# Kernel tuning notes

Hardware: AMD Instinct MI355X
Metric: run time of the kernel (lower is better)

## Reference

```python
import jax, jax.numpy as jnp
import numpy as np

B, M, N = 2, 256, 256
K, P, Q, D = 8, 512, 512, 64
R, Pp, Qp, Dp = 128, 512, 512, 64
TEMP = float(np.sqrt(Dp))  # softmax temperature = sqrt(D')


def _xavier(key, shape):
    # xavier_uniform over last two dims (fan_in, fan_out), matching torch init on (K, d, D)
    fan_in, fan_out = shape[-2], shape[-1]
    lim = float(np.sqrt(6.0 / (fan_in + fan_out)))
    return jax.random.uniform(key, shape, jnp.float32, -lim, lim)


def setup_inputs() -> dict:
    key = jax.random.key(0)
    ks = jax.random.split(key, 9)
    return {
        "z": jax.random.normal(ks[0], (B, M, N, R), jnp.float32),
        "y_q": jax.random.normal(ks[1], (B, N, Qp), jnp.float32),
        "x_k": jax.random.normal(ks[2], (B, M, Pp), jnp.float32),
        "Theta_x": _xavier(ks[3], (K, P, D)),
        "Theta_y": _xavier(ks[4], (K, Q, D)),
        "Lam_x": _xavier(ks[5], (K, Pp, Dp)),
        "Lam_y": _xavier(ks[6], (K, Qp, Dp)),
        "Lam_zx": _xavier(ks[7], (K, R, Dp)),
        "Lam_zy": _xavier(ks[8], (K, R, Dp)),
    }


def reference(z, y_q, x_k, Theta_x, Theta_y, Lam_x, Lam_y, Lam_zx, Lam_zy):
    # --- mixed attention scores ---
    xt = jnp.einsum('bmp,kpd->bkmd', x_k, Lam_x)          # [B,K,M,D']
    yt = jnp.einsum('bnq,kqd->bknd', y_q, Lam_y)          # [B,K,N,D']
    r = jnp.einsum('bkmd,bknd->bkmn', xt, yt)             # pairwise term
    zy = jnp.einsum('bmnr,krd->bkmnd', z, Lam_zy)         # [B,K,M,N,D'] (large)
    r = r + jnp.einsum('bkmnd,bkmd->bkmn', zy, xt)
    r = r + jnp.einsum('bknd,bmnr,krd->bkmn', yt, z, Lam_zx)
    # --- generalised convolution (mask=None, bias=False) ---
    a = jax.nn.softmax(r / TEMP, axis=-2)                 # softmax over M (column-wise)
    xv = jnp.einsum('bmp,kpd->bkmd', x_k, Theta_x)        # value projection
    y = jnp.einsum('bkmn,bkmd,kqd->bnq', a, xv, Theta_y)  # [B,N,Q]
    return y
```

## Files before the change

### kernel.cpp

```cpp
#include <hip/hip_runtime.h>
#include <hip/hip_bf16.h>

#define LOG2E_OVER_T 0.18033688011112042f

typedef __attribute__((ext_vector_type(8))) short short8;
typedef __attribute__((ext_vector_type(4))) float f32x4;
typedef unsigned short ushort_t;
typedef unsigned long long ull_t;

#define MFMA16(a, b, c) __builtin_amdgcn_mfma_f32_16x16x32_bf16(a, b, c, 0, 0, 0)

__device__ __forceinline__ ushort_t f2bf(float f) {
    union { float f; unsigned u; } v; v.f = f;
    unsigned r = (v.u + 0x7fffu + ((v.u >> 16) & 1u)) >> 16;
    return (ushort_t)r;
}

__device__ __forceinline__ void gload16(const float* g, float* l) {
    __builtin_amdgcn_global_load_lds(
        (const __attribute__((address_space(1))) void*)g,
        (__attribute__((address_space(3))) void*)l, 16, 0, 0);
}

__device__ __forceinline__ void split8(const float4 a, const float4 b,
                                       short8& hi, short8& lo)
{
    union { float f[8]; unsigned u[8]; } Z;
    Z.f[0] = a.x; Z.f[1] = a.y; Z.f[2] = a.z; Z.f[3] = a.w;
    Z.f[4] = b.x; Z.f[5] = b.y; Z.f[6] = b.z; Z.f[7] = b.w;
    union { unsigned u[4]; short8 s; } H, L;
    #pragma unroll
    for (int i = 0; i < 4; i++) {
        const unsigned u0 = Z.u[2 * i], u1 = Z.u[2 * i + 1];
        H.u[i] = __builtin_amdgcn_perm(u1, u0, 0x07060302u);
        union { unsigned u; float f; } h0, h1;
        h0.u = u0 & 0xffff0000u; h1.u = u1 & 0xffff0000u;
        union { float f; unsigned u; } l0, l1;
        l0.f = Z.f[2 * i] - h0.f; l1.f = Z.f[2 * i + 1] - h1.f;
        L.u[i] = __builtin_amdgcn_perm(l1.u, l0.u, 0x07060302u);
    }
    hi = H.s; lo = L.s;
}

__device__ __forceinline__ void mfma_core64(
    const ushort_t* __restrict__ Ag, int lda,
    const ushort_t* __restrict__ Btg, int ldb,
    int ksteps, f32x4 acc[2][2])
{
    __shared__ __align__(16) ushort_t As[64 * 40];
    __shared__ __align__(16) ushort_t Bs[64 * 40];
    const int t = threadIdx.x;
    const int srow = t >> 2, skc = (t & 3) * 8;
    const int lane = t & 63, w = t >> 6;
    const int wr = w >> 1, wc = w & 1;
    const int fr = lane & 15, kg = lane >> 4;
    const int aoff = (wr * 32 + fr) * 40 + kg * 8;
    const int boff = (wc * 32 + fr) * 40 + kg * 8;
    const long arow = (long)srow * lda + skc;
    const long brow = (long)srow * ldb + skc;

    short8 ra = *(const short8*)(Ag + arow);
    short8 rb = *(const short8*)(Btg + brow);
    for (int kt = 0; kt < ksteps; kt++) {
        __syncthreads();
        *(short8*)&As[srow * 40 + skc] = ra;
        *(short8*)&Bs[srow * 40 + skc] = rb;
        __syncthreads();
        if (kt + 1 < ksteps) {
            ra = *(const short8*)(Ag + arow + (kt + 1) * 32);
            rb = *(const short8*)(Btg + brow + (kt + 1) * 32);
        }
        short8 a0 = *(const short8*)&As[aoff];
        short8 a1 = *(const short8*)&As[aoff + 16 * 40];
        short8 b0 = *(const short8*)&Bs[boff];
        short8 b1 = *(const short8*)&Bs[boff + 16 * 40];
        acc[0][0] = MFMA16(a0, b0, acc[0][0]);
        acc[0][1] = MFMA16(a0, b1, acc[0][1]);
        acc[1][0] = MFMA16(a1, b0, acc[1][0]);
        acc[1][1] = MFMA16(a1, b1, acc[1][1]);
    }
}

__device__ __forceinline__ void zero_acc(f32x4 acc[2][2]) {
    const f32x4 z4 = {0.f, 0.f, 0.f, 0.f};
    acc[0][0] = z4; acc[0][1] = z4; acc[1][0] = z4; acc[1][1] = z4;
}

__global__ __launch_bounds__(256)
void convert_kernel(const float* __restrict__ x_k, const float* __restrict__ y_q,
                    const float* __restrict__ Lam_x, const float* __restrict__ Theta_x,
                    const float* __restrict__ Lam_y, const float* __restrict__ Lam_zy,
                    const float* __restrict__ Lam_zx, const float* __restrict__ Theta_y,
                    ushort_t* __restrict__ xkb, ushort_t* __restrict__ yqb,
                    ushort_t* __restrict__ WxTb, ushort_t* __restrict__ WyTb,
                    ushort_t* __restrict__ Zyb, ushort_t* __restrict__ Zxb,
                    ushort_t* __restrict__ TyTb, float* __restrict__ ssum)
{
    int i = blockIdx.x * 256 + threadIdx.x;
    if (i < 262144) { xkb[i] = f2bf(x_k[i]); return; }
    i -= 262144;
    if (i < 262144) { yqb[i] = f2bf(y_q[i]); return; }
    i -= 262144;
    if (i < 524288) {
        const int k = i >> 16, rem = i & 65535, dc = rem >> 9, p = i & 511;
        const float v = (dc < 64) ? Lam_x[((long)k * 512 + p) * 64 + dc]
                                  : Theta_x[((long)k * 512 + p) * 64 + dc - 64];
        WxTb[i] = f2bf(v); return;
    }
    i -= 524288;
    if (i < 262144) {
        const int k = i >> 15, d = (i >> 9) & 63, p = i & 511;
        WyTb[i] = f2bf(Lam_y[((long)k * 512 + p) * 64 + d]); return;
    }
    i -= 262144;
    if (i < 65536) { Zyb[i] = f2bf(Lam_zy[i]); return; }
    i -= 65536;
    if (i < 65536) { Zxb[i] = f2bf(Lam_zx[i]); return; }
    i -= 65536;
    if (i < 262144) {
        const int q = i >> 9, kd = i & 511, k = kd >> 6, d = kd & 63;
        TyTb[i] = f2bf(Theta_y[((long)k * 512 + q) * 64 + d]); return;
    }
    i -= 262144;
    ssum[i] = 0.f;
}

__global__ __launch_bounds__(256)
void proj_kernel(const ushort_t* __restrict__ xkb, const ushort_t* __restrict__ yqb,
                 const ushort_t* __restrict__ WxTb, const ushort_t* __restrict__ WyTb,
                 ushort_t* __restrict__ xtb, ushort_t* __restrict__ ytb,
                 ushort_t* __restrict__ xvTb)
{
    const int side = blockIdx.z;
    const int bx = blockIdx.x, by = blockIdx.y;
    if (side == 1 && bx >= 8) return;
    f32x4 acc[2][2]; zero_acc(acc);
    const int t = threadIdx.x, lane = t & 63, w = t >> 6;
    const int wr = w >> 1, wc = w & 1, fr = lane & 15, kg = lane >> 4;

    if (side == 0) {
        mfma_core64(xkb + (long)(by * 64) * 512, 512,
                    WxTb + (long)(bx * 64) * 512, 512, 16, acc);
        const int k = bx >> 1, isxv = bx & 1;
        #pragma unroll
        for (int mi = 0; mi < 2; mi++)
        #pragma unroll
        for (int ni = 0; ni < 2; ni++) {
            const int grow0 = by * 64 + wr * 32 + mi * 16 + kg * 4;
            const int b = grow0 >> 8, m0 = grow0 & 255;
            const int d = wc * 32 + ni * 16 + fr;
            if (!isxv) {
                #pragma unroll
                for (int j = 0; j < 4; j++)
                    xtb[(((long)(b * 8 + k)) * 256 + m0 + j) * 64 + d] = f2bf(acc[mi][ni][j]);
            } else {
                ull_t pk = (ull_t)f2bf(acc[mi][ni][0])
                         | ((ull_t)f2bf(acc[mi][ni][1]) << 16)
                         | ((ull_t)f2bf(acc[mi][ni][2]) << 32)
                         | ((ull_t)f2bf(acc[mi][ni][3]) << 48);
                *(ull_t*)&xvTb[(((long)(b * 8 + k)) * 64 + d) * 256 + m0] = pk;
            }
        }
    } else {
        mfma_core64(yqb + (long)(by * 64) * 512, 512,
                    WyTb + (long)(bx * 64) * 512, 512, 16, acc);
        const int k = bx;
        #pragma unroll
        for (int mi = 0; mi < 2; mi++)
        #pragma unroll
        for (int ni = 0; ni < 2; ni++)
        #pragma unroll
        for (int j = 0; j < 4; j++) {
            const int grow = by * 64 + wr * 32 + mi * 16 + kg * 4 + j;
            const int b = grow >> 8, n = grow & 255;
            const int d = wc * 32 + ni * 16 + fr;
            ytb[(((long)(b * 8 + k)) * 256 + n) * 64 + d] = f2bf(acc[mi][ni][j]);
        }
    }
}

__global__ __launch_bounds__(256)
void step2_kernel(const ushort_t* __restrict__ xtb, const ushort_t* __restrict__ ytb,
                  const ushort_t* __restrict__ Zyb, const ushort_t* __restrict__ Zxb,
                  ushort_t* __restrict__ wzyb, ushort_t* __restrict__ wzxb,
                  float* __restrict__ t1)
{
    const int bz = blockIdx.x;
    const int t = threadIdx.x, lane = t & 63, w = t >> 6;
    const int wr = w >> 1, wc = w & 1, fr = lane & 15, kg = lane >> 4;

    if (bz < 256) {
        const int which = bz >> 7, idx = bz & 127;
        const int bk = idx >> 3, tile = idx & 7, mt = tile >> 1, nt = tile & 1;
        const int k = bk & 7, b = bk >> 3;
        const ushort_t* Ag  = (which ? ytb : xtb) + ((long)bk * 256 + mt * 64) * 64;
        const ushort_t* Btg = (which ? Zxb : Zyb) + ((long)k * 128 + nt * 64) * 64;
        ushort_t* C = which ? wzxb : wzyb;
        f32x4 acc[2][2]; zero_acc(acc);
        mfma_core64(Ag, 64, Btg, 64, 2, acc);
        #pragma unroll
        for (int mi = 0; mi < 2; mi++)
        #pragma unroll
        for (int ni = 0; ni < 2; ni++)
        #pragma unroll
        for (int j = 0; j < 4; j++) {
            const int m_glob = mt * 64 + wr * 32 + mi * 16 + kg * 4 + j;
            const int r_glob = nt * 64 + wc * 32 + ni * 16 + fr;
            C[(((long)b * 256 + m_glob) * 8 + k) * 128 + r_glob] = f2bf(acc[mi][ni][j]);
        }
    } else {
        const int idx = bz - 256;
        const int bk = idx >> 4, tile = idx & 15, nt2 = tile >> 2, mt2 = tile & 3;
        f32x4 acc[2][2]; zero_acc(acc);
        mfma_core64(ytb + ((long)bk * 256 + nt2 * 64) * 64, 64,
                    xtb + ((long)bk * 256 + mt2 * 64) * 64, 64, 2, acc);
        #pragma unroll
        for (int mi = 0; mi < 2; mi++)
        #pragma unroll
        for (int ni = 0; ni < 2; ni++)
        #pragma unroll
        for (int j = 0; j < 4; j++) {
            const int n_glob = nt2 * 64 + wr * 32 + mi * 16 + kg * 4 + j;
            const int m_glob = mt2 * 64 + wc * 32 + ni * 16 + fr;
            t1[((long)bk * 256 + n_glob) * 256 + m_glob] = acc[mi][ni][j];
        }
    }
}

__global__ __launch_bounds__(256)
void fused_score(const float* __restrict__ z,
                 const ushort_t* __restrict__ wzyb, const ushort_t* __restrict__ wzxb,
                 const float* __restrict__ t1, ushort_t* __restrict__ Et,
                 float* __restrict__ ssum)
{
    const int nt = blockIdx.x, mt = blockIdx.y, b = blockIdx.z;
    const int nbase = nt * 16, m0 = mt * 8;
    __shared__ __align__(16) float zs[8192];
    __shared__ float sc[4][8][8][17];

    const int tid = threadIdx.x;
    const int lane = tid & 63, w = tid >> 6;
    const int fr = lane & 15, kg = lane >> 4;
    const int f8 = fr & 7;

    const int js   = w * 512 + lane;
    for (int c = 0; c < 2; c++) {
        const int n0c = nbase + c * 8;

        #pragma unroll
        for (int i = 0; i < 8; i++) {
            const int j   = js + i * 64;
            const int row = j >> 5;
            const int m_l = row >> 3, n_l = row & 7;
            const int sl  = (j & 31) ^ ((m_l ^ n_l) & 7);
            const float* src = z + (((long)b * 256 + m0 + m_l) * 256 + n0c + n_l) * 128 + sl * 4;
            gload16(src, &zs[(w * 8 + i) * 256]);
        }
        __syncthreads();

        #pragma unroll
        for (int m = 0; m < 8; m++) {
            const int row = m * 8 + f8;
            const int key = (m ^ f8) & 7;
            const int s0 = (w * 8 + kg * 2) ^ key, s1 = (w * 8 + kg * 2 + 1) ^ key;
            const float4 za = *(const float4*)&zs[row * 128 + s0 * 4];
            const float4 zb = *(const float4*)&zs[row * 128 + s1 * 4];
            const short8 wv = *(const short8*)(wzyb
                + (((long)b * 256 + m0 + m) * 8 + f8) * 128 + w * 32 + kg * 8);
            short8 hi, lo;
            split8(za, zb, hi, lo);
            f32x4 acc = {0.f, 0.f, 0.f, 0.f};
            acc = MFMA16(hi, wv, acc);
            acc = MFMA16(lo, wv, acc);
            if (fr < 8 && kg < 2) {
                #pragma unroll
                for (int j = 0; j < 4; j++)
                    sc[w][m][fr][c * 8 + kg * 4 + j] = acc[j];
            }
        }

        #pragma unroll
        for (int nl = 0; nl < 8; nl++) {
            const int row = f8 * 8 + nl;
            const int key = (f8 ^ nl) & 7;
            const int s0 = (w * 8 + kg * 2) ^ key, s1 = (w * 8 + kg * 2 + 1) ^ key;
            const float4 za = *(const float4*)&zs[row * 128 + s0 * 4];
            const float4 zb = *(const float4*)&zs[row * 128 + s1 * 4];
            const short8 wv = *(const short8*)(wzxb
                + (((long)b * 256 + n0c + nl) * 8 + f8) * 128 + w * 32 + kg * 8);
            short8 hi, lo;
            split8(za, zb, hi, lo);
            f32x4 acc = {0.f, 0.f, 0.f, 0.f};
            acc = MFMA16(hi, wv, acc);
            acc = MFMA16(lo, wv, acc);
            if (fr < 8 && kg < 2) {
                #pragma unroll
                for (int j = 0; j < 4; j++)
                    sc[w][kg * 4 + j][fr][c * 8 + nl] += acc[j];
            }
        }
        __syncthreads();
    }

    if (tid < 128) {
        const int k = tid >> 4, n = tid & 15;
        const float* tp = t1 + (((long)b * 8 + k) * 256 + nbase + n) * 256 + m0;
        const float4 t0 = *(const float4*)(tp);
        const float4 t4 = *(const float4*)(tp + 4);
        const float tv[8] = {t0.x, t0.y, t0.z, t0.w, t4.x, t4.y, t4.z, t4.w};
        float s8 = 0.f;
        ushort_t eb[8];
        #pragma unroll
        for (int m = 0; m < 8; m++) {
            const float s = sc[0][m][k][n] + sc[1][m][k][n]
                          + sc[2][m][k][n] + sc[3][m][k][n] + tv[m];
            const float e = exp2f(s * LOG2E_OVER_T);
            eb[m] = f2bf(e);
            s8 += e;
        }
        *(short8*)(Et + (((long)b * 8 + k) * 256 + nbase + n) * 256 + m0) = *(short8*)eb;
        atomicAdd(&ssum[(b * 8 + k) * 256 + nbase + n], s8);
    }
}

__global__ __launch_bounds__(256)
void ogemm_kernel(const ushort_t* __restrict__ Et, const ushort_t* __restrict__ xvTb,
                  const float* __restrict__ ssum, ushort_t* __restrict__ o2b)
{
    const int mt = blockIdx.x, bk = blockIdx.y;
    f32x4 acc[2][2]; zero_acc(acc);
    mfma_core64(Et + ((long)bk * 256 + mt * 64) * 256, 256,
                xvTb + (long)bk * 64 * 256, 256, 8, acc);
    const int t = threadIdx.x, lane = t & 63, w = t >> 6;
    const int wr = w >> 1, wc = w & 1, fr = lane & 15, kg = lane >> 4;
    const int b = bk >> 3, k = bk & 7;
    #pragma unroll
    for (int mi = 0; mi < 2; mi++)
    #pragma unroll
    for (int j = 0; j < 4; j++) {
        const int n = mt * 64 + wr * 32 + mi * 16 + kg * 4 + j;
        const float inv = 1.0f / ssum[bk * 256 + n];
        #pragma unroll
        for (int ni = 0; ni < 2; ni++) {
            const int d = wc * 32 + ni * 16 + fr;
            o2b[((long)b * 256 + n) * 512 + k * 64 + d] = f2bf(acc[mi][ni][j] * inv);
        }
    }
}

__global__ __launch_bounds__(256)
void ygemm_kernel(const ushort_t* __restrict__ o2b, const ushort_t* __restrict__ TyTb,
                  float* __restrict__ out)
{
    const int qt = blockIdx.x, mt = blockIdx.y, b = blockIdx.z;
    f32x4 acc[2][2]; zero_acc(acc);
    mfma_core64(o2b + ((long)b * 256 + mt * 64) * 512, 512,
                TyTb + (long)qt * 64 * 512, 512, 16, acc);
    const int t = threadIdx.x, lane = t & 63, w = t >> 6;
    const int wr = w >> 1, wc = w & 1, fr = lane & 15, kg = lane >> 4;
    #pragma unroll
    for (int mi = 0; mi < 2; mi++)
    #pragma unroll
    for (int ni = 0; ni < 2; ni++)
    #pragma unroll
    for (int j = 0; j < 4; j++) {
        const int n = mt * 64 + wr * 32 + mi * 16 + kg * 4 + j;
        const int q = qt * 64 + wc * 32 + ni * 16 + fr;
        out[((long)b * 256 + n) * 512 + q] = acc[mi][ni][j];
    }
}

extern "C" void kernel_launch(void* const* d_in, const int* in_sizes, int n_in,
                              void* d_out, int out_size, void* d_ws, size_t ws_size,
                              hipStream_t stream)
{
    const float* z       = (const float*)d_in[0];
    const float* y_q     = (const float*)d_in[1];
    const float* x_k     = (const float*)d_in[2];
    const float* Theta_x = (const float*)d_in[3];
    const float* Theta_y = (const float*)d_in[4];
    const float* Lam_x   = (const float*)d_in[5];
    const float* Lam_y   = (const float*)d_in[6];
    const float* Lam_zx  = (const float*)d_in[7];
    const float* Lam_zy  = (const float*)d_in[8];
    float* out = (float*)d_out;

    ushort_t* U = (ushort_t*)d_ws;
    ushort_t* xkb  = U;
    ushort_t* yqb  = U + 262144;
    ushort_t* WxTb = U + 524288;
    ushort_t* WyTb = U + 1048576;
    ushort_t* Zyb  = U + 1310720;
    ushort_t* Zxb  = U + 1376256;
    ushort_t* TyTb = U + 1441792;
    ushort_t* xtb  = U + 1703936;
    ushort_t* ytb  = U + 1966080;
    ushort_t* xvTb = U + 2228224;
    ushort_t* wzyb = U + 2490368;
    ushort_t* wzxb = U + 3014656;
    ushort_t* Et   = U + 3538944;
    ushort_t* o2b  = U + 4587520;
    float*    ssum = (float*)(U + 4849664);
    float*    t1   = (float*)(U + 4857856);

    convert_kernel<<<6672, 256, 0, stream>>>(x_k, y_q, Lam_x, Theta_x, Lam_y,
        Lam_zy, Lam_zx, Theta_y, xkb, yqb, WxTb, WyTb, Zyb, Zxb, TyTb, ssum);

    proj_kernel<<<dim3(16, 8, 2), 256, 0, stream>>>(xkb, yqb, WxTb, WyTb,
        xtb, ytb, xvTb);

    step2_kernel<<<512, 256, 0, stream>>>(xtb, ytb, Zyb, Zxb, wzyb, wzxb, t1);

    fused_score<<<dim3(16, 32, 2), 256, 0, stream>>>(z, wzyb, wzxb, t1,
        Et, ssum);

    ogemm_kernel<<<dim3(4, 16), 256, 0, stream>>>(Et, xvTb, ssum, o2b);

    ygemm_kernel<<<dim3(8, 4, 2), 256, 0, stream>>>(o2b, TyTb, out);
}
```

Before: 58.93 us.

## Stage wzy/wzx weights in LDS with swizzled layout and double fused_score waves

step2 now writes the wzy/wzx bf16 weights in a tile-blocked, XOR-swizzled layout. fused_score can then load them into LDS with async global_load_lds instead of strided per-lane global reads. fused_score now runs 512 threads with two half-blocks that each take one n-chunk, so the two-iteration loop and one barrier go away. The cost is much more LDS per block (64KB z plus 64KB of weights), which likely limits occupancy to one block per CU.

```diff
diff --git a/kernel.cpp b/kernel.cpp
--- a/kernel.cpp
+++ b/kernel.cpp
@@ -16,7 +16,7 @@
     return (ushort_t)r;
 }
 
-__device__ __forceinline__ void gload16(const float* g, float* l) {
+__device__ __forceinline__ void gload16(const void* g, void* l) {
     __builtin_amdgcn_global_load_lds(
         (const __attribute__((address_space(1))) void*)g,
         (__attribute__((address_space(3))) void*)l, 16, 0, 0);
@@ -204,9 +204,13 @@
         for (int ni = 0; ni < 2; ni++)
         #pragma unroll
         for (int j = 0; j < 4; j++) {
-            const int m_glob = mt * 64 + wr * 32 + mi * 16 + kg * 4 + j;
-            const int r_glob = nt * 64 + wc * 32 + ni * 16 + fr;
-            C[(((long)b * 256 + m_glob) * 8 + k) * 128 + r_glob] = f2bf(acc[mi][ni][j]);
+            const int ent = mt * 64 + wr * 32 + mi * 16 + kg * 4 + j;
+            const int r_g = nt * 64 + wc * 32 + ni * 16 + fr;
+            const int t8 = ent >> 3, lo = ent & 7;
+            const int wq = r_g >> 5, q = (r_g >> 3) & 3, e = r_g & 7;
+            const int phys = q ^ (k & 3);
+            C[((((long)(b * 32 + t8)) * 4 + wq) * 64 + lo * 8 + k) * 32 + phys * 8 + e]
+                = f2bf(acc[mi][ni][j]);
         }
     } else {
         const int idx = bz - 256;
@@ -227,7 +231,7 @@
     }
 }
 
-__global__ __launch_bounds__(256)
+__global__ __launch_bounds__(512)
 void fused_score(const float* __restrict__ z,
                  const ushort_t* __restrict__ wzyb, const ushort_t* __restrict__ wzxb,
                  const float* __restrict__ t1, ushort_t* __restrict__ Et,
@@ -235,72 +239,82 @@
 {
     const int nt = blockIdx.x, mt = blockIdx.y, b = blockIdx.z;
     const int nbase = nt * 16, m0 = mt * 8;
-    __shared__ __align__(16) float zs[8192];
-    __shared__ float sc[4][8][8][17];
+    __shared__ __align__(16) float    zs[16384];
+    __shared__ __align__(16) ushort_t wyl[16384];
+    __shared__ __align__(16) ushort_t wxl[16384];
+    __shared__ float sc[4][8][8][16];
 
     const int tid = threadIdx.x;
-    const int lane = tid & 63, w = tid >> 6;
+    const int lane = tid & 63, wv = tid >> 6;
+    const int w = wv & 3, h = wv >> 2;
     const int fr = lane & 15, kg = lane >> 4;
     const int f8 = fr & 7;
-
-    const int js   = w * 512 + lane;
-    for (int c = 0; c < 2; c++) {
-        const int n0c = nbase + c * 8;
-
-        #pragma unroll
-        for (int i = 0; i < 8; i++) {
-            const int j   = js + i * 64;
-            const int row = j >> 5;
-            const int m_l = row >> 3, n_l = row & 7;
-            const int sl  = (j & 31) ^ ((m_l ^ n_l) & 7);
-            const float* src = z + (((long)b * 256 + m0 + m_l) * 256 + n0c + n_l) * 128 + sl * 4;
-            gload16(src, &zs[(w * 8 + i) * 256]);
-        }
-        __syncthreads();
-
-        #pragma unroll
-        for (int m = 0; m < 8; m++) {
-            const int row = m * 8 + f8;
-            const int key = (m ^ f8) & 7;
-            const int s0 = (w * 8 + kg * 2) ^ key, s1 = (w * 8 + kg * 2 + 1) ^ key;
-            const float4 za = *(const float4*)&zs[row * 128 + s0 * 4];
-            const float4 zb = *(const float4*)&zs[row * 128 + s1 * 4];
-            const short8 wv = *(const short8*)(wzyb
-                + (((long)b * 256 + m0 + m) * 8 + f8) * 128 + w * 32 + kg * 8);
-            short8 hi, lo;
-            split8(za, zb, hi, lo);
-            f32x4 acc = {0.f, 0.f, 0.f, 0.f};
-            acc = MFMA16(hi, wv, acc);
-            acc = MFMA16(lo, wv, acc);
-            if (fr < 8 && kg < 2) {
-                #pragma unroll
-                for (int j = 0; j < 4; j++)
-                    sc[w][m][fr][c * 8 + kg * 4 + j] = acc[j];
-            }
-        }
-
-        #pragma unroll
-        for (int nl = 0; nl < 8; nl++) {
-            const int row = f8 * 8 + nl;
-            const int key = (f8 ^ nl) & 7;
-            const int s0 = (w * 8 + kg * 2) ^ key, s1 = (w * 8 + kg * 2 + 1) ^ key;
-            const float4 za = *(const float4*)&zs[row * 128 + s0 * 4];
-            const float4 zb = *(const float4*)&zs[row * 128 + s1 * 4];
-            const short8 wv = *(const short8*)(wzxb
-                + (((long)b * 256 + n0c + nl) * 8 + f8) * 128 + w * 32 + kg * 8);
-            short8 hi, lo;
-            split8(za, zb, hi, lo);
-            f32x4 acc = {0.f, 0.f, 0.f, 0.f};
-            acc = MFMA16(hi, wv, acc);
-            acc = MFMA16(lo, wv, acc);
-            if (fr < 8 && kg < 2) {
-                #pragma unroll
-                for (int j = 0; j < 4; j++)
-                    sc[w][kg * 4 + j][fr][c * 8 + nl] += acc[j];
-            }
-        }
-        __syncthreads();
-    }
+    const int reg = h * 4 + w;
+    const int kg2 = kg * 2;
+
+    {
+        const ushort_t* src = wzyb + (((long)(b * 32 + mt)) * 4 + w) * 2048;
+        #pragma unroll
+        for (int j = 0; j < 4; j++)
+            gload16(src + j * 512 + lane * 8, &wyl[reg * 2048 + j * 512]);
+    }
+    {
+        const ushort_t* src = wzxb + (((long)(b * 32 + nt * 2 + h)) * 4 + w) * 2048;
+        #pragma unroll
+        for (int j = 0; j < 4; j++)
+            gload16(src + j * 512 + lane * 8, &wxl[reg * 2048 + j * 512]);
+    }
+    #pragma unroll
+    for (int i = 0; i < 8; i++) {
+        const int rr = i * 8 + (lane >> 3);
+        const int m_l = rr >> 3, n_l = rr & 7;
+        const int key = (m_l ^ n_l) & 7;
+        const float* src = z + (((long)b * 256 + m0 + m_l) * 256 + nbase + h * 8 + n_l) * 128
+                             + w * 32 + (((lane & 7) ^ key)) * 4;
+        gload16(src, &zs[reg * 2048 + i * 256]);
+    }
+
+    asm volatile("s_waitcnt vmcnt(0)" ::: "memory");
+    __builtin_amdgcn_sched_barrier(0);
+
+    #pragma unroll
+    for (int m = 0; m < 8; m++) {
+        const int row = m * 8 + f8;
+        const int key = (m ^ f8) & 7;
+        const float4 za = *(const float4*)&zs[reg * 2048 + row * 32 + ((kg2) ^ key) * 4];
+        const float4 zb = *(const float4*)&zs[reg * 2048 + row * 32 + ((kg2 + 1) ^ key) * 4];
+        const short8 wvv = *(const short8*)&wyl[reg * 2048 + row * 32 + (kg ^ (f8 & 3)) * 8];
+        short8 hi, lo;
+        split8(za, zb, hi, lo);
+        f32x4 acc = {0.f, 0.f, 0.f, 0.f};
+        acc = MFMA16(hi, wvv, acc);
+        acc = MFMA16(lo, wvv, acc);
+        if (fr < 8 && kg < 2) {
+            #pragma unroll
+            for (int j = 0; j < 4; j++)
+                sc[w][m][fr][h * 8 + kg * 4 + j] = acc[j];
+        }
+    }
+
+    #pragma unroll
+    for (int nl = 0; nl < 8; nl++) {
+        const int row = f8 * 8 + nl;
+        const int key = (f8 ^ nl) & 7;
+        const float4 za = *(const float4*)&zs[reg * 2048 + row * 32 + ((kg2) ^ key) * 4];
+        const float4 zb = *(const float4*)&zs[reg * 2048 + row * 32 + ((kg2 + 1) ^ key) * 4];
+        const short8 wvv = *(const short8*)&wxl[reg * 2048 + (nl * 8 + f8) * 32 + (kg ^ (f8 & 3)) * 8];
+        short8 hi, lo;
+        split8(za, zb, hi, lo);
+        f32x4 acc = {0.f, 0.f, 0.f, 0.f};
+        acc = MFMA16(hi, wvv, acc);
+        acc = MFMA16(lo, wvv, acc);
+        if (fr < 8 && kg < 2) {
+            #pragma unroll
+            for (int j = 0; j < 4; j++)
+                sc[w][kg * 4 + j][fr][h * 8 + nl] += acc[j];
+        }
+    }
+    __syncthreads();
 
     if (tid < 128) {
         const int k = tid >> 4, n = tid & 15;
@@ -411,7 +425,7 @@
 
     step2_kernel<<<512, 256, 0, stream>>>(xtb, ytb, Zyb, Zxb, wzyb, wzxb, t1);
 
-    fused_score<<<dim3(16, 32, 2), 256, 0, stream>>>(z, wzyb, wzxb, t1,
+    fused_score<<<dim3(16, 32, 2), 512, 0, stream>>>(z, wzyb, wzxb, t1,
         Et, ssum);
 
     ogemm_kernel<<<dim3(4, 16), 256, 0, stream>>>(Et, xvTb, ssum, o2b);
```

New measurement: 62.91 us. +6.7%, slower.
